# Kernel optimization log

Hardware: AMD Instinct MI355X
Metric: run time of the kernel (lower is better)

The kernel has to match this reference:

```python
import jax, jax.numpy as jnp
import numpy as np

WIN = 7
NUM_HEADS = 4
HEAD_DIM = 32  # 128 / 4


def _relative_position_index(win=WIN):
    coords = np.stack(np.meshgrid(np.arange(win), np.arange(win), indexing='ij'))  # [2,w,w]
    coords = coords.reshape(2, -1)  # [2, w*w]
    rel = coords[:, :, None] - coords[:, None, :]  # [2, ws, ws]
    rel = rel.transpose(1, 2, 0)  # [ws, ws, 2]
    idx = (rel[..., 0] + win - 1) * (2 * win - 1) + (rel[..., 1] + win - 1)
    return jnp.asarray(idx, dtype=jnp.int32)  # [49, 49]


def setup_inputs() -> dict:
    key = jax.random.key(0)
    ks = jax.random.split(key, 6)
    B, S, D = 4096, WIN * WIN, 128
    nW = 64  # windows per image
    return {
        'hidden_states': jax.random.normal(ks[0], (B, S, D), dtype=jnp.float32),
        'attention_mask': jnp.zeros((nW, S, S), dtype=jnp.float32),
        'Wq': jax.random.normal(ks[1], (D, D), dtype=jnp.float32) * 0.02,
        'bq': jnp.zeros((D,), dtype=jnp.float32),
        'Wk': jax.random.normal(ks[2], (D, D), dtype=jnp.float32) * 0.02,
        'bk': jnp.zeros((D,), dtype=jnp.float32),
        'Wv': jax.random.normal(ks[3], (D, D), dtype=jnp.float32) * 0.02,
        'bv': jnp.zeros((D,), dtype=jnp.float32),
        'bias_table': jax.random.normal(ks[4], ((2 * WIN - 1) ** 2, NUM_HEADS), dtype=jnp.float32) * 0.02,
    }


def reference(hidden_states, attention_mask, Wq, bq, Wk, bk, Wv, bv, bias_table):
    B, S, D = hidden_states.shape
    H, Dh = NUM_HEADS, HEAD_DIM

    def heads(x):  # [B,S,D] -> [B,H,S,Dh]
        return x.reshape(B, S, H, Dh).transpose(0, 2, 1, 3)

    q = heads(hidden_states @ Wq + bq)
    k = heads(hidden_states @ Wk + bk)
    v = heads(hidden_states @ Wv + bv)

    scores = jnp.einsum('bhqd,bhkd->bhqk', q, k) / np.sqrt(Dh).astype(np.float32)

    idx = _relative_position_index()  # [S,S] int32 constant
    rel_bias = bias_table[idx]  # [S,S,H]
    scores = scores + rel_bias.transpose(2, 0, 1)[None]  # [B,H,S,S]

    nW = attention_mask.shape[0]
    scores = scores.reshape(B // nW, nW, H, S, S) + attention_mask[None, :, None]
    scores = scores.reshape(B, H, S, S)

    probs = jax.nn.softmax(scores, axis=-1)
    ctx = jnp.einsum('bhqk,bhkd->bhqd', probs, v)
    return ctx.transpose(0, 2, 1, 3).reshape(B, S, D)
```

## Files before the change

kernel.cpp:

```cpp
#include <hip/hip_runtime.h>
#include <hip/hip_bf16.h>

#define S49 49
#define D128 128
#define NH 4

typedef __attribute__((ext_vector_type(8))) short short8;
typedef __attribute__((ext_vector_type(4))) short short4v;
typedef __attribute__((ext_vector_type(4))) float f32x4;

__device__ __forceinline__ unsigned short f2b(float x){
  unsigned u = __builtin_bit_cast(unsigned, x);
  return (unsigned short)((u + 0x7fffu + ((u>>16)&1u)) >> 16);
}
__device__ __forceinline__ unsigned pk2(float a, float b){
  __hip_bfloat162 h = __float22bfloat162_rn(float2{a, b});
  unsigned u; __builtin_memcpy(&u, &h, 4);
  return u;
}
__device__ __forceinline__ int swz256i(int row, int col){
  return row*128 + ((((col>>3) ^ (row&15)) << 3) | (col&7));
}

__global__ void prep_wt(const float* __restrict__ Wq, const float* __restrict__ Wk,
                        const float* __restrict__ Wv, unsigned short* __restrict__ wt){
  int e = blockIdx.x*256 + threadIdx.x;
  if (e >= 3*128*128) return;
  int mat = e >> 14, rem = e & 16383, n = rem >> 7, k = rem & 127;
  const float* W = (mat==0) ? Wq : ((mat==1) ? Wk : Wv);
  wt[e] = f2b(W[k*128 + n]);
}

__global__ void prep_comb(const float* __restrict__ mask, const float* __restrict__ bt,
                          float4* __restrict__ comb4, int nW){
  int e = blockIdx.x*256 + threadIdx.x;
  if (e >= nW*NH*S49*16) return;
  int ln = e & 15; int t = e >> 4;
  int i = t % S49; t /= S49;
  int h = t & (NH-1); int w = t / NH;
  const float* mrow = mask + ((size_t)w*S49 + i)*S49;
  int ri = i/7, ci = i - ri*7;
  const float L2E = 1.4426950408889634f;
  float v[4];
  #pragma unroll
  for (int nt = 0; nt < 4; ++nt){
    int j = nt*16 + ln;
    if (j < S49){
      int rj = j/7, cj = j - rj*7;
      int idx = (ri - rj + 6)*13 + (ci - cj + 6);
      v[nt] = (mrow[j] + bt[idx*NH + h]) * L2E;
    } else v[nt] = -1e30f;
  }
  float4 o; o.x = v[0]; o.y = v[1]; o.z = v[2]; o.w = v[3];
  comb4[e] = o;
}

__global__ __launch_bounds__(512, 6) void swin_attn(
    const float* __restrict__ hs,
    const float* __restrict__ bq, const float* __restrict__ bk,
    const float* __restrict__ bv,
    const float4* __restrict__ comb4,
    const unsigned short* __restrict__ wt, float* __restrict__ out, int nW){

  __shared__ __align__(16) unsigned short lds[26832];
  unsigned short* hs_s = lds;
  unsigned short* q_s  = lds + 6272;
  unsigned short* k_s  = lds + 12544;
  unsigned short* vt_s = lds + 18816;
  unsigned short* pext = lds + 25984;

  const int b = blockIdx.x;
  const int tid = threadIdx.x;
  const int wave = tid >> 6, lane = tid & 63;
  const int lg = lane >> 4, ln = lane & 15;
  unsigned short* pp = (wave < 7) ? (hs_s + wave*832) : pext;

  const float* hsb = hs + (size_t)b * (S49*D128);
  #pragma unroll
  for (int it = 0; it < 4; ++it) {
    int u = tid + it*512;
    if (u < S49*32) {
      int row = u >> 5, c = u & 31;
      float4 f = *(const float4*)(hsb + row*128 + c*4);
      uint2 o; o.x = pk2(f.x, f.y); o.y = pk2(f.z, f.w);
      *(uint2*)&hs_s[swz256i(row, c*4)] = o;
    }
  }
  if (tid < 128) {
    uint2 z2 = {0u,0u};
    *(uint2*)&vt_s[tid*56 + 48] = z2;
    *(uint2*)&vt_s[tid*56 + 52] = z2;
  }
  __syncthreads();

  const int w = b % nW;
  const int rt = wave & 3, hp = wave >> 2;
  const int mbw = (rt<3) ? rt*16 : 33;

  {
    const int ntb = wave*16;
    #pragma unroll 1
    for (int mat = 0; mat < 3; ++mat) {
      short8 a[4];
      #pragma unroll
      for (int ks = 0; ks < 4; ++ks)
        a[ks] = *(const short8*)&wt[(mat<<14) + (ntb+ln)*128 + ks*32 + lg*8];
      const float* bp = (mat==0) ? bq : ((mat==1) ? bk : bv);
      float4 bias = *(const float4*)&bp[ntb + 4*lg];
      #pragma unroll
      for (int mt = 0; mt < 4; ++mt) {
        const int mb = (mt<3) ? mt*16 : 33;
        short8 bh[4];
        #pragma unroll
        for (int ks = 0; ks < 4; ++ks)
          bh[ks] = *(const short8*)&hs_s[swz256i(mb+ln, ks*32 + lg*8)];
        f32x4 acc = {0.f,0.f,0.f,0.f};
        #pragma unroll
        for (int ks = 0; ks < 4; ++ks)
          acc = __builtin_amdgcn_mfma_f32_16x16x32_bf16(a[ks], bh[ks], acc, 0,0,0);
        const int m = mb + ln;
        const int nb = ntb + 4*lg;
        if (mat == 0) {
          uint2 o; o.x = pk2(acc[0]+bias.x, acc[1]+bias.y);
                   o.y = pk2(acc[2]+bias.z, acc[3]+bias.w);
          *(uint2*)&q_s[swz256i(m, nb)] = o;
        } else if (mat == 1) {
          uint2 o; o.x = pk2(acc[0]+bias.x, acc[1]+bias.y);
                   o.y = pk2(acc[2]+bias.z, acc[3]+bias.w);
          *(uint2*)&k_s[swz256i(m, nb)] = o;
        } else {
          vt_s[(nb+0)*56 + m] = f2b(acc[0]+bias.x);
          vt_s[(nb+1)*56 + m] = f2b(acc[1]+bias.y);
          vt_s[(nb+2)*56 + m] = f2b(acc[2]+bias.z);
          vt_s[(nb+3)*56 + m] = f2b(acc[3]+bias.w);
        }
      }
    }
  }
  __syncthreads();

  const float C1 = 0.17677669529663687f * 1.4426950408889634f;
  const short8 ones = {16256,16256,16256,16256,16256,16256,16256,16256};
  const short4v z4 = {0,0,0,0};

  #pragma unroll
  for (int hh = 0; hh < 2; ++hh) {
    const int h = hp*2 + hh;
    float4 cb[4];
    #pragma unroll
    for (int r = 0; r < 4; ++r)
      cb[r] = comb4[((size_t)(w*NH + h)*S49 + mbw + 4*lg + r)*16 + ln];

    short8 aq = *(const short8*)&q_s[swz256i(mbw+ln, h*32 + lg*8)];
    short8 kb[4];
    #pragma unroll
    for (int nt = 0; nt < 4; ++nt)
      kb[nt] = *(const short8*)&k_s[swz256i(nt*16+ln, h*32 + lg*8)];
    if (ln != 0) kb[3] = short8{0,0,0,0,0,0,0,0};
    f32x4 s[4];
    __builtin_amdgcn_s_setprio(1);
    #pragma unroll
    for (int nt = 0; nt < 4; ++nt) {
      f32x4 z = {0.f,0.f,0.f,0.f};
      s[nt] = __builtin_amdgcn_mfma_f32_16x16x32_bf16(aq, kb[nt], z, 0,0,0);
    }
    __builtin_amdgcn_s_setprio(0);

    #pragma unroll
    for (int r = 0; r < 4; ++r) {
      float cbv[4] = {cb[r].x, cb[r].y, cb[r].z, cb[r].w};
      #pragma unroll
      for (int nt = 0; nt < 4; ++nt) {
        float e = __builtin_amdgcn_exp2f(fmaf(s[nt][r], C1, cbv[nt]));
        if (nt < 3 || ln < 4)
          pp[(4*lg + r)*52 + nt*16 + ln] = f2b(e);
      }
    }

    short4v a0 = *(const short4v*)&pp[ln*52 + lg*8];
    short4v a1 = *(const short4v*)&pp[ln*52 + lg*8 + 4];
    short8 ap0 = __builtin_shufflevector(a0, a1, 0,1,2,3,4,5,6,7);
    short4v b0 = *(const short4v*)&pp[ln*52 + 32 + lg*8];
    short4v b1 = *(const short4v*)&pp[ln*52 + 36 + lg*8];
    if (lg >= 2) b1 = z4;
    if (lg == 3) b0 = z4;
    short8 ap1 = __builtin_shufflevector(b0, b1, 0,1,2,3,4,5,6,7);

    f32x4 sacc = {0.f,0.f,0.f,0.f};
    __builtin_amdgcn_s_setprio(1);
    sacc = __builtin_amdgcn_mfma_f32_16x16x32_bf16(ap0, ones, sacc, 0,0,0);
    sacc = __builtin_amdgcn_mfma_f32_16x16x32_bf16(ap1, ones, sacc, 0,0,0);
    __builtin_amdgcn_s_setprio(0);
    float inv[4];
    #pragma unroll
    for (int r = 0; r < 4; ++r) inv[r] = __builtin_amdgcn_rcpf(sacc[r]);

    #pragma unroll
    for (int nt = 0; nt < 2; ++nt) {
      const int vr = h*32 + nt*16 + ln;
      short8 bv0 = *(const short8*)&vt_s[vr*56 + lg*8];
      short8 bv1 = {0,0,0,0,0,0,0,0};
      if (lg < 3) bv1 = *(const short8*)&vt_s[vr*56 + 32 + lg*8];
      f32x4 acc = {0.f,0.f,0.f,0.f};
      __builtin_amdgcn_s_setprio(1);
      acc = __builtin_amdgcn_mfma_f32_16x16x32_bf16(ap0, bv0, acc, 0,0,0);
      acc = __builtin_amdgcn_mfma_f32_16x16x32_bf16(ap1, bv1, acc, 0,0,0);
      __builtin_amdgcn_s_setprio(0);
      const int mr = mbw + 4*lg;
      #pragma unroll
      for (int r = 0; r < 4; ++r)
        out[((size_t)b*S49 + mr + r)*D128 + vr] = acc[r]*inv[r];
    }
  }
}

extern "C" void kernel_launch(void* const* d_in, const int* in_sizes, int n_in,
                              void* d_out, int out_size, void* d_ws, size_t ws_size,
                              hipStream_t stream){
  const float* hs  = (const float*)d_in[0];
  const float* msk = (const float*)d_in[1];
  const float* Wq  = (const float*)d_in[2];
  const float* bq  = (const float*)d_in[3];
  const float* Wk  = (const float*)d_in[4];
  const float* bk  = (const float*)d_in[5];
  const float* Wv  = (const float*)d_in[6];
  const float* bv  = (const float*)d_in[7];
  const float* bt  = (const float*)d_in[8];
  unsigned short* wt = (unsigned short*)d_ws;
  float4* comb4 = (float4*)((char*)d_ws + 98304);
  float* out = (float*)d_out;
  const int B  = in_sizes[0] / (S49*D128);
  const int nW = in_sizes[1] / (S49*S49);
  prep_wt<<<dim3((3*128*128 + 255)/256), dim3(256), 0, stream>>>(Wq, Wk, Wv, wt);
  prep_comb<<<dim3((nW*NH*S49*16 + 255)/256), dim3(256), 0, stream>>>(msk, bt, comb4, nW);
  swin_attn<<<dim3(B), dim3(512), 0, stream>>>(hs, bq, bk, bv, comb4, wt, out, nW);
}
```

Baseline: 92.51 us.

## Compute transposed scores so softmax rows live in lanes, normalize before PV

```diff
diff --git a/kernel.cpp b/kernel.cpp
--- a/kernel.cpp
+++ b/kernel.cpp
@@ -6,7 +6,6 @@
 #define NH 4
 
 typedef __attribute__((ext_vector_type(8))) short short8;
-typedef __attribute__((ext_vector_type(4))) short short4v;
 typedef __attribute__((ext_vector_type(4))) float f32x4;
 
 __device__ __forceinline__ unsigned short f2b(float x){
@@ -35,7 +34,8 @@
                           float4* __restrict__ comb4, int nW){
   int e = blockIdx.x*256 + threadIdx.x;
   if (e >= nW*NH*S49*16) return;
-  int ln = e & 15; int t = e >> 4;
+  int s = e & 15; int nt = s >> 2, lg = s & 3;
+  int t = e >> 4;
   int i = t % S49; t /= S49;
   int h = t & (NH-1); int w = t / NH;
   const float* mrow = mask + ((size_t)w*S49 + i)*S49;
@@ -43,13 +43,13 @@
   const float L2E = 1.4426950408889634f;
   float v[4];
   #pragma unroll
-  for (int nt = 0; nt < 4; ++nt){
-    int j = nt*16 + ln;
+  for (int r = 0; r < 4; ++r){
+    int j = nt*16 + lg*4 + r;
     if (j < S49){
       int rj = j/7, cj = j - rj*7;
       int idx = (ri - rj + 6)*13 + (ci - cj + 6);
-      v[nt] = (mrow[j] + bt[idx*NH + h]) * L2E;
-    } else v[nt] = -1e30f;
+      v[r] = (mrow[j] + bt[idx*NH + h]) * L2E;
+    } else v[r] = -1e30f;
   }
   float4 o; o.x = v[0]; o.y = v[1]; o.z = v[2]; o.w = v[3];
   comb4[e] = o;
@@ -62,7 +62,7 @@
     const float4* __restrict__ comb4,
     const unsigned short* __restrict__ wt, float* __restrict__ out, int nW){
 
-  __shared__ __align__(16) unsigned short lds[26832];
+  __shared__ __align__(16) unsigned short lds[26880];
   unsigned short* hs_s = lds;
   unsigned short* q_s  = lds + 6272;
   unsigned short* k_s  = lds + 12544;
@@ -73,7 +73,7 @@
   const int tid = threadIdx.x;
   const int wave = tid >> 6, lane = tid & 63;
   const int lg = lane >> 4, ln = lane & 15;
-  unsigned short* pp = (wave < 7) ? (hs_s + wave*832) : pext;
+  unsigned short* pp = (wave < 7) ? (hs_s + wave*896) : pext;
 
   const float* hsb = hs + (size_t)b * (S49*D128);
   #pragma unroll
@@ -140,66 +140,64 @@
   __syncthreads();
 
   const float C1 = 0.17677669529663687f * 1.4426950408889634f;
-  const short8 ones = {16256,16256,16256,16256,16256,16256,16256,16256};
-  const short4v z4 = {0,0,0,0};
+  const short8 z8 = {0,0,0,0,0,0,0,0};
 
   #pragma unroll
   for (int hh = 0; hh < 2; ++hh) {
     const int h = hp*2 + hh;
     float4 cb[4];
     #pragma unroll
-    for (int r = 0; r < 4; ++r)
-      cb[r] = comb4[((size_t)(w*NH + h)*S49 + mbw + 4*lg + r)*16 + ln];
+    for (int nt = 0; nt < 4; ++nt)
+      cb[nt] = comb4[((size_t)((w*NH + h)*S49) + mbw + ln)*16 + nt*4 + lg];
 
     short8 aq = *(const short8*)&q_s[swz256i(mbw+ln, h*32 + lg*8)];
     short8 kb[4];
     #pragma unroll
     for (int nt = 0; nt < 4; ++nt)
       kb[nt] = *(const short8*)&k_s[swz256i(nt*16+ln, h*32 + lg*8)];
-    if (ln != 0) kb[3] = short8{0,0,0,0,0,0,0,0};
-    f32x4 s[4];
+    if (ln != 0) kb[3] = z8;
+    f32x4 st[4];
     __builtin_amdgcn_s_setprio(1);
     #pragma unroll
     for (int nt = 0; nt < 4; ++nt) {
       f32x4 z = {0.f,0.f,0.f,0.f};
-      s[nt] = __builtin_amdgcn_mfma_f32_16x16x32_bf16(aq, kb[nt], z, 0,0,0);
+      st[nt] = __builtin_amdgcn_mfma_f32_16x16x32_bf16(kb[nt], aq, z, 0,0,0);
     }
     __builtin_amdgcn_s_setprio(0);
 
-    #pragma unroll
-    for (int r = 0; r < 4; ++r) {
-      float cbv[4] = {cb[r].x, cb[r].y, cb[r].z, cb[r].w};
-      #pragma unroll
-      for (int nt = 0; nt < 4; ++nt) {
-        float e = __builtin_amdgcn_exp2f(fmaf(s[nt][r], C1, cbv[nt]));
-        if (nt < 3 || ln < 4)
-          pp[(4*lg + r)*52 + nt*16 + ln] = f2b(e);
+    float e[4][4], psum[4];
+    #pragma unroll
+    for (int nt = 0; nt < 4; ++nt) {
+      float cbv[4] = {cb[nt].x, cb[nt].y, cb[nt].z, cb[nt].w};
+      #pragma unroll
+      for (int r = 0; r < 4; ++r)
+        e[nt][r] = __builtin_amdgcn_exp2f(fmaf(st[nt][r], C1, cbv[r]));
+      psum[nt] = (e[nt][0] + e[nt][1]) + (e[nt][2] + e[nt][3]);
+    }
+    float sum = (psum[0] + psum[1]) + (psum[2] + psum[3]);
+    sum += __shfl_xor(sum, 16, 64);
+    sum += __shfl_xor(sum, 32, 64);
+    const float inv = __builtin_amdgcn_rcpf(sum);
+
+    #pragma unroll
+    for (int nt = 0; nt < 4; ++nt) {
+      #pragma unroll
+      for (int rp = 0; rp < 2; ++rp) {
+        if (nt < 3 || lg < 2) {
+          unsigned u = pk2(e[nt][2*rp]*inv, e[nt][2*rp+1]*inv);
+          *(unsigned*)&pp[ln*56 + nt*16 + lg*4 + 2*rp] = u;
+        }
       }
     }
 
-    short4v a0 = *(const short4v*)&pp[ln*52 + lg*8];
-    short4v a1 = *(const short4v*)&pp[ln*52 + lg*8 + 4];
-    short8 ap0 = __builtin_shufflevector(a0, a1, 0,1,2,3,4,5,6,7);
-    short4v b0 = *(const short4v*)&pp[ln*52 + 32 + lg*8];
-    short4v b1 = *(const short4v*)&pp[ln*52 + 36 + lg*8];
-    if (lg >= 2) b1 = z4;
-    if (lg == 3) b0 = z4;
-    short8 ap1 = __builtin_shufflevector(b0, b1, 0,1,2,3,4,5,6,7);
-
-    f32x4 sacc = {0.f,0.f,0.f,0.f};
-    __builtin_amdgcn_s_setprio(1);
-    sacc = __builtin_amdgcn_mfma_f32_16x16x32_bf16(ap0, ones, sacc, 0,0,0);
-    sacc = __builtin_amdgcn_mfma_f32_16x16x32_bf16(ap1, ones, sacc, 0,0,0);
-    __builtin_amdgcn_s_setprio(0);
-    float inv[4];
-    #pragma unroll
-    for (int r = 0; r < 4; ++r) inv[r] = __builtin_amdgcn_rcpf(sacc[r]);
-
+    short8 ap0 = *(const short8*)&pp[ln*56 + lg*8];
+    short8 ap1 = z8;
+    if (lg < 3) ap1 = *(const short8*)&pp[ln*56 + 32 + lg*8];
     #pragma unroll
     for (int nt = 0; nt < 2; ++nt) {
       const int vr = h*32 + nt*16 + ln;
       short8 bv0 = *(const short8*)&vt_s[vr*56 + lg*8];
-      short8 bv1 = {0,0,0,0,0,0,0,0};
+      short8 bv1 = z8;
       if (lg < 3) bv1 = *(const short8*)&vt_s[vr*56 + 32 + lg*8];
       f32x4 acc = {0.f,0.f,0.f,0.f};
       __builtin_amdgcn_s_setprio(1);
@@ -209,7 +207,7 @@
       const int mr = mbw + 4*lg;
       #pragma unroll
       for (int r = 0; r < 4; ++r)
-        out[((size_t)b*S49 + mr + r)*D128 + vr] = acc[r]*inv[r];
+        out[((size_t)b*S49 + mr + r)*D128 + vr] = acc[r];
     }
   }
 }
```

New measurement: 109.2 us. +18.1%, slower.
